# Kernel optimization log

Measured on AMD Instinct MI355X. Metric: run time of the kernel, lower is better.

## Reference

```python
import jax, jax.numpy as jnp
import numpy as np

N_HEADS = 12
LN_EPS = 1e-12


def _attention(x, mask, wq, bq, wk, bk, wv, bv, wo, bo):
    # standard BERT self-attention block (QKV + output projection, no LN here)
    B, S, D = x.shape
    Dh = D // N_HEADS
    q = (x @ wq + bq).reshape(B, S, N_HEADS, Dh)
    k = (x @ wk + bk).reshape(B, S, N_HEADS, Dh)
    v = (x @ wv + bv).reshape(B, S, N_HEADS, Dh)
    scores = jnp.einsum('bqhd,bkhd->bhqk', q, k) / jnp.sqrt(jnp.asarray(Dh, x.dtype))
    scores = scores + mask[:, None, None, :]  # additive mask, broadcast over heads/queries
    a = jax.nn.softmax(scores, axis=-1)
    ctx = jnp.einsum('bhqk,bkhd->bqhd', a, v).reshape(B, S, D)
    return ctx @ wo + bo


def _ffn(x, w1, b1, w2, b2):
    return jax.nn.gelu(x @ w1 + b1, approximate=False) @ w2 + b2


def _switch_ffn(x, wr, br, w1, b1, w2, b2):
    # token-level top-1 Switch FFN: route each token, scale output by max route prob.
    # All sub-experts are computed densely and combined with a one-hot mask so the
    # math is identical to gather/scatter dispatch but jit-friendly.
    B, S, D = x.shape
    E = wr.shape[-1]
    tok = x.reshape(-1, D)  # [N, D]
    p = jax.nn.softmax(tok @ wr + br, axis=-1)  # [N, E]
    pmax = p.max(axis=-1)
    oh = jax.nn.one_hot(p.argmax(axis=-1), E, dtype=tok.dtype)  # [N, E]
    h = jax.nn.gelu(jnp.einsum('nd,edf->enf', tok, w1) + b1[:, None, :], approximate=False)
    y = jnp.einsum('enf,efd->end', h, w2) + b2[:, None, :]  # [E, N, D]
    out = jnp.einsum('ne,end->nd', oh, y) * pmax[:, None]
    return out.reshape(B, S, D)


def setup_inputs() -> dict:
    B, S, D, F, U, E = 16, 128, 768, 3072, 4, 4
    key = jax.random.key(0)
    ks = jax.random.split(key, 20)
    w = lambda i, sh: jax.random.normal(ks[i], sh, dtype=jnp.float32) * 0.02
    z = lambda sh: jnp.zeros(sh, jnp.float32)
    return {
        'x': jax.random.normal(ks[0], (B, S, D), jnp.float32),
        'attn_mask': z((B, S)),
        'sw_w': w(1, (D, U)), 'sw_b': z((U,)),
        'ca_wq': w(2, (D, D)), 'ca_bq': z((D,)),
        'ca_wk': w(3, (D, D)), 'ca_bk': z((D,)),
        'ca_wv': w(4, (D, D)), 'ca_bv': z((D,)),
        'ca_wo': w(5, (D, D)), 'ca_bo': z((D,)),
        'ua_wq': w(6, (U, D, D)), 'ua_bq': z((U, D)),
        'ua_wk': w(7, (U, D, D)), 'ua_bk': z((U, D)),
        'ua_wv': w(8, (U, D, D)), 'ua_bv': z((U, D)),
        'ua_wo': w(9, (U, D, D)), 'ua_bo': z((U, D)),
        'cf_w1': w(10, (D, F)), 'cf_b1': z((F,)),
        'cf_w2': w(11, (F, D)), 'cf_b2': z((D,)),
        'ur_w': w(12, (U, D, E)), 'ur_b': z((U, E)),
        'uf_w1': w(13, (U, E, D, F)), 'uf_b1': z((U, E, F)),
        'uf_w2': w(14, (U, E, F, D)), 'uf_b2': z((U, E, D)),
        'ln_g': jnp.ones((D,), jnp.float32), 'ln_b': z((D,)),
    }


def reference(x, attn_mask, sw_w, sw_b,
              ca_wq, ca_bq, ca_wk, ca_bk, ca_wv, ca_bv, ca_wo, ca_bo,
              ua_wq, ua_bq, ua_wk, ua_bk, ua_wv, ua_bv, ua_wo, ua_bo,
              cf_w1, cf_b1, cf_w2, cf_b2,
              ur_w, ur_b, uf_w1, uf_b1, uf_w2, uf_b2,
              ln_g, ln_b):
    U = sw_w.shape[-1]
    # common attention expert (full batch)
    common_attn = _attention(x, attn_mask, ca_wq, ca_bq, ca_wk, ca_bk, ca_wv, ca_bv, ca_wo, ca_bo)
    # batch-level routing: mean-pool over sequence, softmax + top-1
    route_p = jax.nn.softmax(x.mean(axis=1) @ sw_w + sw_b, axis=-1)  # [B, U]
    pmax = route_p.max(axis=-1)    # [B]
    routes = route_p.argmax(axis=-1)  # [B]
    # unique attention experts: masked dense compute == gather/scatter by batch row
    unique_attn = jnp.zeros_like(x)
    for i in range(U):
        sel = (routes == i)[:, None, None]
        out_i = _attention(x, attn_mask, ua_wq[i], ua_bq[i], ua_wk[i], ua_bk[i],
                           ua_wv[i], ua_bv[i], ua_wo[i], ua_bo[i])
        unique_attn = unique_attn + jnp.where(sel, out_i, jnp.zeros((), x.dtype))
    # note: original multiplies ONLY the unique branch by route_prob_max
    att = common_attn + pmax[:, None, None] * unique_attn
    # unique Switch-FFN experts (token-level top-1 inside each unique expert)
    unique_ffn = jnp.zeros_like(x)
    for i in range(U):
        sel = (routes == i)[:, None, None]
        out_i = _switch_ffn(att, ur_w[i], ur_b[i], uf_w1[i], uf_b1[i], uf_w2[i], uf_b2[i])
        unique_ffn = unique_ffn + jnp.where(sel, out_i, jnp.zeros((), x.dtype))
    common_ffn = _ffn(att, cf_w1, cf_b1, cf_w2, cf_b2)
    ffn_out = common_ffn + unique_ffn  # dropout in eval mode == identity
    y = att + ffn_out
    mu = y.mean(axis=-1, keepdims=True)
    var = y.var(axis=-1, keepdims=True)
    return (y - mu) / jnp.sqrt(var + LN_EPS) * ln_g + ln_b
```

## Files before the change

kernel.cpp:

```cpp
#include <hip/hip_runtime.h>

#define NT 2048
#define Dm 768
#define Fm 3072
#define Bm 16
#define Sm 128
#define Hm 12
#define DHm 64

#define BM 64
#define BM2 128
#define BN 128
#define BK 32

typedef __attribute__((ext_vector_type(8))) short bf16x8;
typedef __attribute__((ext_vector_type(4))) float f32x4;

__device__ __forceinline__ unsigned short f2bf(float f){
  unsigned u = __float_as_uint(f);
  unsigned r = (u + 0x7fffu + ((u>>16)&1u)) >> 16;
  return (unsigned short)r;
}
__device__ __forceinline__ float bf2f(unsigned short h){ return __uint_as_float(((unsigned)h)<<16); }
__device__ __forceinline__ unsigned fsplit2(float x){
  unsigned short h = f2bf(x);
  unsigned short l = f2bf(x - bf2f(h));
  return (unsigned)h | ((unsigned)l << 16);
}
__device__ __forceinline__ void bsplit2(float a, float b, unsigned &hi2, unsigned &lo2){
  asm("v_cvt_pk_bf16_f32 %0, %1, %2" : "=v"(hi2) : "v"(a), "v"(b));
  float fa = __uint_as_float(hi2 << 16);
  float fb = __uint_as_float(hi2 & 0xffff0000u);
  asm("v_cvt_pk_bf16_f32 %0, %1, %2" : "=v"(lo2) : "v"(a - fa), "v"(b - fb));
}
__device__ __forceinline__ float gelu_f(float x){
  return 0.5f*x*(1.0f + erff(x*0.70710678118654752f));
}

__device__ __forceinline__ void mm_tile2(
    const short* __restrict__ Abf, int lda,
    const int* __restrict__ gidx, int m0, int mbound,
    const float* __restrict__ W0, int N, int K, int n0,
    f32x4 acc[4][4])
{
  int lane = threadIdx.x & 63, wv = threadIdx.x >> 6;
  int wm = wv & 1, wn = wv >> 1;
  int oct = lane >> 4, l16 = lane & 15;
  const short* aptr[4];
  #pragma unroll
  for(int fi=0; fi<4; fi++){
    int lr = wm*64 + fi*16 + l16;
    int grow = (lr < mbound) ? (gidx ? gidx[m0 + lr] : (m0 + lr)) : -1;
    aptr[fi] = (grow >= 0) ? (Abf + (size_t)grow*lda + oct*8) : nullptr;
  }
  const float* bptr[4];
  #pragma unroll
  for(int fj=0; fj<4; fj++)
    bptr[fj] = W0 + (size_t)(oct*8)*N + (n0 + wn*64 + fj*16 + l16);

  const bf16x8 zz = {0,0,0,0,0,0,0,0};
  bf16x8 av[4]; float bw[4][8];
  #pragma unroll
  for(int fi=0; fi<4; fi++) av[fi] = aptr[fi] ? *(const bf16x8*)(aptr[fi]) : zz;
  #pragma unroll
  for(int fj=0; fj<4; fj++)
    #pragma unroll
    for(int i=0;i<8;i++) bw[fj][i] = bptr[fj][(size_t)i*N];

  for(int k0=0; k0<K; k0+=BK){
    bf16x8 af[4];
    #pragma unroll
    for(int fi=0; fi<4; fi++) af[fi] = av[fi];
    bf16x8 bfr[4];
    #pragma unroll
    for(int fj=0; fj<4; fj++){
      unsigned o0,o1,o2,o3;
      asm("v_cvt_pk_bf16_f32 %0, %1, %2" : "=v"(o0) : "v"(bw[fj][0]), "v"(bw[fj][1]));
      asm("v_cvt_pk_bf16_f32 %0, %1, %2" : "=v"(o1) : "v"(bw[fj][2]), "v"(bw[fj][3]));
      asm("v_cvt_pk_bf16_f32 %0, %1, %2" : "=v"(o2) : "v"(bw[fj][4]), "v"(bw[fj][5]));
      asm("v_cvt_pk_bf16_f32 %0, %1, %2" : "=v"(o3) : "v"(bw[fj][6]), "v"(bw[fj][7]));
      union{ bf16x8 v; unsigned u[4]; } r;
      r.u[0]=o0; r.u[1]=o1; r.u[2]=o2; r.u[3]=o3;
      bfr[fj] = r.v;
    }
    if(k0+BK < K){
      int kn = k0 + BK;
      #pragma unroll
      for(int fi=0; fi<4; fi++) av[fi] = aptr[fi] ? *(const bf16x8*)(aptr[fi] + kn) : zz;
      #pragma unroll
      for(int fj=0; fj<4; fj++)
        #pragma unroll
        for(int i=0;i<8;i++) bw[fj][i] = bptr[fj][(size_t)(kn + i)*N];
    }
    __builtin_amdgcn_s_setprio(1);
    #pragma unroll
    for(int fi=0; fi<4; fi++)
      #pragma unroll
      for(int fj=0; fj<4; fj++)
        acc[fi][fj] = __builtin_amdgcn_mfma_f32_16x16x32_bf16(af[fi], bfr[fj], acc[fi][fj], 0, 0, 0);
    __builtin_amdgcn_s_setprio(0);
  }
}

__device__ __forceinline__ void mm_tile3b(
    const short* __restrict__ Ahi, const short* __restrict__ Alo, int lda, int m0, int acol,
    const float* __restrict__ W0, int N, int K, int n0,
    f32x4 acc[2][4])
{
  int lane = threadIdx.x & 63, wv = threadIdx.x >> 6;
  int wm = wv & 1, wn = wv >> 1;
  int oct = lane >> 4, l16 = lane & 15;
  size_t aoffs[2];
  #pragma unroll
  for(int fi=0; fi<2; fi++){
    int lr = wm*32 + fi*16 + l16;
    aoffs[fi] = (size_t)(m0 + lr)*lda + acol + oct*8;
  }
  const float* bptr[4];
  #pragma unroll
  for(int fj=0; fj<4; fj++)
    bptr[fj] = W0 + (size_t)(oct*8)*N + (n0 + wn*64 + fj*16 + l16);

  bf16x8 avH[2], avL[2]; float bw[4][8];
  #pragma unroll
  for(int fi=0; fi<2; fi++){
    avH[fi] = *(const bf16x8*)(Ahi + aoffs[fi]);
    avL[fi] = *(const bf16x8*)(Alo + aoffs[fi]);
  }
  #pragma unroll
  for(int fj=0; fj<4; fj++)
    #pragma unroll
    for(int i=0;i<8;i++) bw[fj][i] = bptr[fj][(size_t)i*N];

  for(int k0=0; k0<K; k0+=BK){
    bf16x8 ah[2], al[2];
    #pragma unroll
    for(int fi=0; fi<2; fi++){ ah[fi]=avH[fi]; al[fi]=avL[fi]; }
    bf16x8 bh[4], bl[4];
    #pragma unroll
    for(int fj=0; fj<4; fj++){
      unsigned h0,l0,h1,l1,h2,l2,h3,l3;
      bsplit2(bw[fj][0], bw[fj][1], h0, l0);
      bsplit2(bw[fj][2], bw[fj][3], h1, l1);
      bsplit2(bw[fj][4], bw[fj][5], h2, l2);
      bsplit2(bw[fj][6], bw[fj][7], h3, l3);
      union{ bf16x8 v; unsigned u[4]; } rh, rl;
      rh.u[0]=h0; rh.u[1]=h1; rh.u[2]=h2; rh.u[3]=h3;
      rl.u[0]=l0; rl.u[1]=l1; rl.u[2]=l2; rl.u[3]=l3;
      bh[fj] = rh.v; bl[fj] = rl.v;
    }
    if(k0+BK < K){
      int kn = k0 + BK;
      #pragma unroll
      for(int fi=0; fi<2; fi++){
        avH[fi] = *(const bf16x8*)(Ahi + aoffs[fi] + kn);
        avL[fi] = *(const bf16x8*)(Alo + aoffs[fi] + kn);
      }
      #pragma unroll
      for(int fj=0; fj<4; fj++)
        #pragma unroll
        for(int i=0;i<8;i++) bw[fj][i] = bptr[fj][(size_t)(kn + i)*N];
    }
    __builtin_amdgcn_s_setprio(1);
    #pragma unroll
    for(int fi=0; fi<2; fi++)
      #pragma unroll
      for(int fj=0; fj<4; fj++){
        acc[fi][fj] = __builtin_amdgcn_mfma_f32_16x16x32_bf16(ah[fi], bh[fj], acc[fi][fj], 0, 0, 0);
        acc[fi][fj] = __builtin_amdgcn_mfma_f32_16x16x32_bf16(ah[fi], bl[fj], acc[fi][fj], 0, 0, 0);
        acc[fi][fj] = __builtin_amdgcn_mfma_f32_16x16x32_bf16(al[fi], bh[fj], acc[fi][fj], 0, 0, 0);
      }
    __builtin_amdgcn_s_setprio(0);
  }
}

__global__ __launch_bounds__(256) void k_split_x(const float* __restrict__ in,
    short* __restrict__ hi, short* __restrict__ lo, int n4){
  int i = blockIdx.x*256 + threadIdx.x;
  if(i < n4){
    float4 v = ((const float4*)in)[i];
    unsigned h01,l01,h23,l23;
    bsplit2(v.x, v.y, h01, l01);
    bsplit2(v.z, v.w, h23, l23);
    short4 h, l;
    h.x=(short)(h01&0xffff); h.y=(short)(h01>>16); h.z=(short)(h23&0xffff); h.w=(short)(h23>>16);
    l.x=(short)(l01&0xffff); l.y=(short)(l01>>16); l.z=(short)(l23&0xffff); l.w=(short)(l23>>16);
    ((short4*)hi)[i] = h;
    ((short4*)lo)[i] = l;
  }
}

struct PtrArr6 { const float* w[6]; const float* b[6]; };

__global__ __launch_bounds__(256) void mm3_qkv(const short* __restrict__ x_hi,
    const short* __restrict__ x_lo, PtrArr6 pa,
    const int* __restrict__ routeb, float* __restrict__ qkvout)
{
  int n0 = blockIdx.x*BN, m0 = blockIdx.y*BM, z = blockIdx.z;
  int bidx = m0 >> 7;
  const float* W = pa.w[z]; const float* bias = pa.b[z];
  if(z >= 3){ int e = routeb[bidx]; W += (size_t)e*Dm*Dm; bias += (size_t)e*Dm; }
  f32x4 acc[2][4] = {};
  mm_tile3b(x_hi, x_lo, Dm, m0, 0, W, Dm, Dm, n0, acc);
  float* outp = qkvout + (size_t)z*NT*Dm;
  int lane = threadIdx.x&63, wv = threadIdx.x>>6, wm = wv&1, wn = wv>>1;
  #pragma unroll
  for(int fi=0; fi<2; fi++)
    #pragma unroll
    for(int fj=0; fj<4; fj++)
      #pragma unroll
      for(int r=0; r<4; r++){
        int row = m0 + wm*32 + fi*16 + ((lane>>4)<<2) + r;
        int col = n0 + wn*64 + fj*16 + (lane&15);
        outp[(size_t)row*Dm + col] = acc[fi][fj][r] + bias[col];
      }
}

__global__ __launch_bounds__(256) void mm3_outproj(const short* __restrict__ ctx_hi,
    const short* __restrict__ ctx_lo,
    const float* __restrict__ ca_wo, const float* __restrict__ ua_wo,
    const float* __restrict__ ca_bo, const float* __restrict__ ua_bo,
    const int* __restrict__ routeb, const float* __restrict__ pmaxb,
    float* __restrict__ att4)
{
  const int KC = Dm/2;
  int n0 = blockIdx.x*BN, m0 = blockIdx.y*BM, kc = blockIdx.z;
  int bidx = m0 >> 7;
  int e = routeb[bidx];
  int uq = kc >> 1, kh = kc & 1;
  const float* Wb = uq ? (ua_wo + (size_t)e*Dm*Dm) : ca_wo;
  const float* W  = Wb + (size_t)kh*KC*Dm;
  int acol = uq*Dm + kh*KC;
  f32x4 acc[2][4] = {};
  mm_tile3b(ctx_hi, ctx_lo, 1536, m0, acol, W, Dm, KC, n0, acc);
  float* outp = att4 + (size_t)kc*NT*Dm;
  int lane = threadIdx.x&63, wv = threadIdx.x>>6, wm = wv&1, wn = wv>>1;
  #pragma unroll
  for(int fi=0; fi<2; fi++)
    #pragma unroll
    for(int fj=0; fj<4; fj++)
      #pragma unroll
      for(int r=0; r<4; r++){
        int row = m0 + wm*32 + fi*16 + ((lane>>4)<<2) + r;
        int col = n0 + wn*64 + fj*16 + (lane&15);
        float bv = 0.f;
        if(kh == 0) bv = uq ? pmaxb[bidx]*ua_bo[(size_t)e*Dm + col] : ca_bo[col];
        outp[(size_t)row*Dm + col] = acc[fi][fj][r] + bv;
      }
}

__global__ __launch_bounds__(256) void k_att_sum(const float* __restrict__ att4,
    float* __restrict__ att, short* __restrict__ attbf, int n4){
  int i = blockIdx.x*256 + threadIdx.x;
  if(i < n4){
    const size_t P4 = (size_t)NT*Dm/4;
    float4 a = ((const float4*)att4)[i];
    float4 b = ((const float4*)att4)[P4 + i];
    float4 c = ((const float4*)att4)[2*P4 + i];
    float4 d = ((const float4*)att4)[3*P4 + i];
    float4 v;
    v.x=a.x+b.x+c.x+d.x; v.y=a.y+b.y+c.y+d.y;
    v.z=a.z+b.z+c.z+d.z; v.w=a.w+b.w+c.w+d.w;
    ((float4*)att)[i] = v;
    short4 o;
    o.x=(short)f2bf(v.x); o.y=(short)f2bf(v.y); o.z=(short)f2bf(v.z); o.w=(short)f2bf(v.w);
    ((short4*)attbf)[i] = o;
  }
}

__global__ __launch_bounds__(256) void mm_fstage(const short* __restrict__ attbf,
    const float* __restrict__ cf_w1, const float* __restrict__ cf_b1,
    const float* __restrict__ uf_w1, const float* __restrict__ uf_b1,
    const int* __restrict__ idxl, const int* __restrict__ gbase, const int* __restrict__ gcnt,
    const int* __restrict__ tlist, const int* __restrict__ ntl,
    short* __restrict__ h, short* __restrict__ hg)
{
  int n0 = blockIdx.x*BN, y = blockIdx.y;
  int lane = threadIdx.x&63, wv = threadIdx.x>>6, wm = wv&1, wn = wv>>1;
  f32x4 acc[4][4] = {};
  if(y < 16){
    int m0 = y*BM2;
    mm_tile2(attbf, Dm, nullptr, m0, BM2, cf_w1, Fm, Dm, n0, acc);
    #pragma unroll
    for(int fi=0; fi<4; fi++)
      #pragma unroll
      for(int fj=0; fj<4; fj++)
        #pragma unroll
        for(int r=0; r<4; r++){
          int row = m0 + wm*64 + fi*16 + ((lane>>4)<<2) + r;
          int col = n0 + wn*64 + fj*16 + (lane&15);
          h[(size_t)row*Fm + col] = (short)f2bf(gelu_f(acc[fi][fj][r] + cf_b1[col]));
        }
  } else {
    int i = y - 16;
    if(i >= ntl[0]) return;
    int v = tlist[i], g = v>>8, t = v&255;
    int cnt = gcnt[g], r0 = t*BM2, pos0 = gbase[g] + r0;
    mm_tile2(attbf, Dm, idxl, pos0, cnt - r0, uf_w1 + (size_t)g*Dm*Fm, Fm, Dm, n0, acc);
    const float* bias = uf_b1 + (size_t)g*Fm;
    #pragma unroll
    for(int fi=0; fi<4; fi++)
      #pragma unroll
      for(int fj=0; fj<4; fj++)
        #pragma unroll
        for(int r=0; r<4; r++){
          int lr = wm*64 + fi*16 + ((lane>>4)<<2) + r;
          if(r0 + lr >= cnt) continue;
          int col = n0 + wn*64 + fj*16 + (lane&15);
          hg[(size_t)(pos0+lr)*Fm + col] = (short)f2bf(gelu_f(acc[fi][fj][r] + bias[col]));
        }
  }
}

__global__ __launch_bounds__(256) void mm_dstage(const short* __restrict__ h,
    const short* __restrict__ hg,
    const float* __restrict__ cf_w2, const float* __restrict__ cf_b2,
    const float* __restrict__ uf_w2, const float* __restrict__ uf_b2,
    const int* __restrict__ idxl, const int* __restrict__ gbase, const int* __restrict__ gcnt,
    const int* __restrict__ tlist, const int* __restrict__ ntl,
    const float* __restrict__ tokp, short* __restrict__ ycf4, short* __restrict__ yuo4)
{
  const int KC = Fm/4;
  int bx = blockIdx.x;
  int n0 = (bx % 6)*BN, kc = bx / 6;
  int y = blockIdx.y;
  int lane = threadIdx.x&63, wv = threadIdx.x>>6, wm = wv&1, wn = wv>>1;
  f32x4 acc[4][4] = {};
  if(y < 16){
    int m0 = y*BM2;
    mm_tile2(h + kc*KC, Fm, nullptr, m0, BM2, cf_w2 + (size_t)kc*KC*Dm, Dm, KC, n0, acc);
    short* outp = ycf4 + (size_t)kc*NT*Dm;
    #pragma unroll
    for(int fi=0; fi<4; fi++)
      #pragma unroll
      for(int fj=0; fj<4; fj++)
        #pragma unroll
        for(int r=0; r<4; r++){
          int row = m0 + wm*64 + fi*16 + ((lane>>4)<<2) + r;
          int col = n0 + wn*64 + fj*16 + (lane&15);
          outp[(size_t)row*Dm + col] = (short)f2bf(acc[fi][fj][r] + (kc==0 ? cf_b2[col] : 0.f));
        }
  } else {
    int i = y - 16;
    if(i >= ntl[0]) return;
    int v = tlist[i], g = v>>8, t = v&255;
    int cnt = gcnt[g], r0 = t*BM2, pos0 = gbase[g] + r0;
    mm_tile2(hg + kc*KC, Fm, nullptr, pos0, cnt - r0,
             uf_w2 + (size_t)g*Fm*Dm + (size_t)kc*KC*Dm, Dm, KC, n0, acc);
    const float* bias = uf_b2 + (size_t)g*Dm;
    short* outp = yuo4 + (size_t)kc*NT*Dm;
    #pragma unroll
    for(int fi=0; fi<4; fi++)
      #pragma unroll
      for(int fj=0; fj<4; fj++)
        #pragma unroll
        for(int r=0; r<4; r++){
          int lr = wm*64 + fi*16 + ((lane>>4)<<2) + r;
          int rm = (r0 + lr < cnt) ? idxl[pos0 + lr] : -1;
          if(rm < 0) continue;
          int col = n0 + wn*64 + fj*16 + (lane&15);
          float vv = acc[fi][fj][r] + (kc==0 ? bias[col] : 0.f);
          outp[(size_t)rm*Dm + col] = (short)f2bf(vv * tokp[rm]);
        }
  }
}

__global__ __launch_bounds__(256) void k_route_batch(const float* __restrict__ xf,
    const float* __restrict__ sw_w, const float* __restrict__ sw_b,
    float* __restrict__ pmax_b, int* __restrict__ route_b){
  int b = blockIdx.x, tid = threadIdx.x;
  __shared__ float xm[Dm];
  for(int d=tid; d<Dm; d+=256){
    float s=0.f;
    const float* xp = xf + ((size_t)b*Sm)*Dm + d;
    for(int ss=0; ss<Sm; ss++) s += xp[(size_t)ss*Dm];
    xm[d] = s*(1.0f/Sm);
  }
  __syncthreads();
  float a0=0,a1=0,a2=0,a3=0;
  for(int d=tid; d<Dm; d+=256){
    float xv = xm[d];
    a0 += xv*sw_w[d*4+0]; a1 += xv*sw_w[d*4+1];
    a2 += xv*sw_w[d*4+2]; a3 += xv*sw_w[d*4+3];
  }
  __shared__ float red[4][256];
  red[0][tid]=a0; red[1][tid]=a1; red[2][tid]=a2; red[3][tid]=a3;
  for(int off=128; off>0; off>>=1){
    __syncthreads();
    if(tid<off){ for(int u=0;u<4;u++) red[u][tid]+=red[u][tid+off]; }
  }
  __syncthreads();
  if(tid==0){
    float l[4]; for(int u=0;u<4;u++) l[u]=red[u][0]+sw_b[u];
    float m=l[0]; int arg=0;
    for(int u=1;u<4;u++) if(l[u]>m){ m=l[u]; arg=u; }
    float s=0; for(int u=0;u<4;u++) s+=expf(l[u]-m);
    pmax_b[b]=1.0f/s;
    route_b[b]=arg;
  }
}

__global__ __launch_bounds__(256) void k_attn_f(const float* __restrict__ qkv,
    const float* __restrict__ mask, const float* __restrict__ pmaxb,
    short* __restrict__ ctx_hi, short* __restrict__ ctx_lo)
{
  int h = blockIdx.x, b = blockIdx.y, z = blockIdx.z;
  int qh = z & 1, kind = z >> 1;
  const float* Q  = qkv + (size_t)(kind*3+0)*NT*Dm;
  const float* Kp = qkv + (size_t)(kind*3+1)*NT*Dm;
  const float* Vp = qkv + (size_t)(kind*3+2)*NT*Dm;
  int tid = threadIdx.x;
  __shared__ float kv[128][68];
  size_t base = ((size_t)b*Sm)*Dm + h*DHm;
  for(int l=tid; l<2048; l+=256){
    int s=l>>4, d4=(l&15)*4;
    *(float4*)&kv[s][d4] = *(const float4*)(Kp + base + (size_t)s*Dm + d4);
  }
  int ql = tid>>2, quarter = tid&3;
  int qi = qh*64 + ql;
  float4 q4[16];
  const float* qp = Q + base + (size_t)qi*Dm;
  #pragma unroll
  for(int j=0;j<16;j++) q4[j] = *(const float4*)(qp + j*4);
  __syncthreads();
  float sc[32];
  #pragma unroll 4
  for(int t=0;t<32;t++){
    int ki = quarter + 4*t;
    float s=0.f;
    #pragma unroll
    for(int j=0;j<16;j++){
      float4 k4 = *(float4*)&kv[ki][j*4];
      s += q4[j].x*k4.x + q4[j].y*k4.y + q4[j].z*k4.z + q4[j].w*k4.w;
    }
    sc[t] = s*0.125f + mask[b*Sm+ki];
  }
  float m = sc[0];
  #pragma unroll
  for(int t=1;t<32;t++) m = fmaxf(m, sc[t]);
  m = fmaxf(m, __shfl_xor(m,1));
  m = fmaxf(m, __shfl_xor(m,2));
  float sum = 0.f;
  #pragma unroll
  for(int t=0;t<32;t++){ sc[t] = expf(sc[t]-m); sum += sc[t]; }
  sum += __shfl_xor(sum,1);
  sum += __shfl_xor(sum,2);
  float inv = 1.0f/sum;
  #pragma unroll
  for(int t=0;t<32;t++) sc[t] *= inv;
  __syncthreads();
  for(int l=tid; l<2048; l+=256){
    int s=l>>4, d4=(l&15)*4;
    *(float4*)&kv[s][d4] = *(const float4*)(Vp + base + (size_t)s*Dm + d4);
  }
  __syncthreads();
  float4 part[16];
  #pragma unroll
  for(int j=0;j<16;j++){ part[j].x=0; part[j].y=0; part[j].z=0; part[j].w=0; }
  #pragma unroll 4
  for(int t=0;t<32;t++){
    int ki = quarter + 4*t;
    float p = sc[t];
    #pragma unroll
    for(int j=0;j<16;j++){
      float4 v4 = *(float4*)&kv[ki][j*4];
      part[j].x += p*v4.x; part[j].y += p*v4.y; part[j].z += p*v4.z; part[j].w += p*v4.w;
    }
  }
  #pragma unroll
  for(int j=0;j<16;j++){
    part[j].x += __shfl_xor(part[j].x,1); part[j].x += __shfl_xor(part[j].x,2);
    part[j].y += __shfl_xor(part[j].y,1); part[j].y += __shfl_xor(part[j].y,2);
    part[j].z += __shfl_xor(part[j].z,1); part[j].z += __shfl_xor(part[j].z,2);
    part[j].w += __shfl_xor(part[j].w,1); part[j].w += __shfl_xor(part[j].w,2);
  }
  float sck = kind ? pmaxb[b] : 1.0f;
  size_t obase = ((size_t)b*Sm + qi)*1536 + kind*Dm + h*DHm;
  #pragma unroll
  for(int jj=0;jj<4;jj++){
    int j = quarter*4 + jj;
    float4 v = part[j];
    v.x *= sck; v.y *= sck; v.z *= sck; v.w *= sck;
    short4 hh, ll;
    unsigned short t0;
    t0=f2bf(v.x); hh.x=(short)t0; ll.x=(short)f2bf(v.x-bf2f(t0));
    t0=f2bf(v.y); hh.y=(short)t0; ll.y=(short)f2bf(v.y-bf2f(t0));
    t0=f2bf(v.z); hh.z=(short)t0; ll.z=(short)f2bf(v.z-bf2f(t0));
    t0=f2bf(v.w); hh.w=(short)t0; ll.w=(short)f2bf(v.w-bf2f(t0));
    *(short4*)(ctx_hi + obase + j*4) = hh;
    *(short4*)(ctx_lo + obase + j*4) = ll;
  }
}

__global__ __launch_bounds__(256) void k_tok_route(const float* __restrict__ att,
    const float* __restrict__ ur_w, const float* __restrict__ ur_b,
    const int* __restrict__ route_b, float* __restrict__ tok_pmax,
    int* __restrict__ tok_e, int* __restrict__ grp_count)
{
  int n = blockIdx.x, tid = threadIdx.x;
  int i = route_b[n>>7];
  const float* w = ur_w + (size_t)i*Dm*4;
  const float* ap = att + (size_t)n*Dm;
  float a0=0,a1=0,a2=0,a3=0;
  for(int d=tid; d<Dm; d+=256){
    float a = ap[d];
    a0 += a*w[d*4+0]; a1 += a*w[d*4+1];
    a2 += a*w[d*4+2]; a3 += a*w[d*4+3];
  }
  __shared__ float red[4][256];
  red[0][tid]=a0; red[1][tid]=a1; red[2][tid]=a2; red[3][tid]=a3;
  for(int off=128; off>0; off>>=1){
    __syncthreads();
    if(tid<off){ for(int u=0;u<4;u++) red[u][tid]+=red[u][tid+off]; }
  }
  __syncthreads();
  if(tid==0){
    float l[4]; for(int u=0;u<4;u++) l[u]=red[u][0]+ur_b[i*4+u];
    float m=l[0]; int arg=0;
    for(int u=1;u<4;u++) if(l[u]>m){ m=l[u]; arg=u; }
    float s=0; for(int u=0;u<4;u++) s+=expf(l[u]-m);
    tok_pmax[n] = 1.0f/s;
    tok_e[n] = arg;
    atomicAdd(&grp_count[i*4+arg], 1);
  }
}

__global__ void k_prefix(const int* __restrict__ cnt, int* __restrict__ base,
                         int* __restrict__ cur, int* __restrict__ tlist, int* __restrict__ ntl){
  if(threadIdx.x==0 && blockIdx.x==0){
    int s=0, nt=0;
    for(int g=0; g<16; g++){
      base[g]=s; cur[g]=s;
      int tg = (cnt[g] + BM2 - 1)/BM2;
      for(int t=0; t<tg; t++){ if(nt<32) tlist[nt++] = (g<<8)|t; }
      s += cnt[g];
    }
    ntl[0] = nt;
  }
}

__global__ void k_scatter(const int* __restrict__ route_b, const int* __restrict__ tok_e,
                          int* __restrict__ cur, int* __restrict__ idxl){
  int n = blockIdx.x*256 + threadIdx.x;
  if(n < NT){
    int g = route_b[n>>7]*4 + tok_e[n];
    int pos = atomicAdd(&cur[g], 1);
    idxl[pos] = n;
  }
}

__global__ __launch_bounds__(256) void k_final_ln(const float* __restrict__ att,
    const short* __restrict__ ycf4, const short* __restrict__ yuo4,
    const float* __restrict__ ln_g, const float* __restrict__ ln_b, float* __restrict__ out)
{
  int n = blockIdx.x, tid = threadIdx.x;
  __shared__ float yb[Dm];
  __shared__ float red[256];
  size_t base = (size_t)n*Dm;
  const size_t P = (size_t)NT*Dm;
  float ps = 0.f;
  for(int d=tid; d<Dm; d+=256){
    float v = att[base+d];
    #pragma unroll
    for(int c=0; c<4; c++){
      v += bf2f((unsigned short)ycf4[c*P + base + d]);
      v += bf2f((unsigned short)yuo4[c*P + base + d]);
    }
    yb[d]=v; ps+=v;
  }
  red[tid]=ps;
  for(int off=128; off>0; off>>=1){ __syncthreads(); if(tid<off) red[tid]+=red[tid+off]; }
  __syncthreads();
  float mu = red[0]*(1.0f/Dm);
  __syncthreads();
  float pv = 0.f;
  for(int d=tid; d<Dm; d+=256){ float t = yb[d]-mu; pv += t*t; }
  red[tid]=pv;
  for(int off=128; off>0; off>>=1){ __syncthreads(); if(tid<off) red[tid]+=red[tid+off]; }
  __syncthreads();
  float var = red[0]*(1.0f/Dm);
  float rstd = rsqrtf(var + 1e-12f);
  for(int d=tid; d<Dm; d+=256){
    out[base+d] = (yb[d]-mu)*rstd*ln_g[d] + ln_b[d];
  }
}

extern "C" void kernel_launch(void* const* d_in, const int* in_sizes, int n_in,
                              void* d_out, int out_size, void* d_ws, size_t ws_size,
                              hipStream_t stream)
{
  const float* x     =(const float*)d_in[0];
  const float* mask  =(const float*)d_in[1];
  const float* sw_w  =(const float*)d_in[2];
  const float* sw_b  =(const float*)d_in[3];
  const float* ca_wq =(const float*)d_in[4];
  const float* ca_bq =(const float*)d_in[5];
  const float* ca_wk =(const float*)d_in[6];
  const float* ca_bk =(const float*)d_in[7];
  const float* ca_wv =(const float*)d_in[8];
  const float* ca_bv =(const float*)d_in[9];
  const float* ca_wo =(const float*)d_in[10];
  const float* ca_bo =(const float*)d_in[11];
  const float* ua_wq =(const float*)d_in[12];
  const float* ua_bq =(const float*)d_in[13];
  const float* ua_wk =(const float*)d_in[14];
  const float* ua_bk =(const float*)d_in[15];
  const float* ua_wv =(const float*)d_in[16];
  const float* ua_bv =(const float*)d_in[17];
  const float* ua_wo =(const float*)d_in[18];
  const float* ua_bo =(const float*)d_in[19];
  const float* cf_w1 =(const float*)d_in[20];
  const float* cf_b1 =(const float*)d_in[21];
  const float* cf_w2 =(const float*)d_in[22];
  const float* cf_b2 =(const float*)d_in[23];
  const float* ur_w  =(const float*)d_in[24];
  const float* ur_b  =(const float*)d_in[25];
  const float* uf_w1 =(const float*)d_in[26];
  const float* uf_b1 =(const float*)d_in[27];
  const float* uf_w2 =(const float*)d_in[28];
  const float* uf_b2 =(const float*)d_in[29];
  const float* ln_g  =(const float*)d_in[30];
  const float* ln_b  =(const float*)d_in[31];

  float* region = (float*)d_ws;
  float* qkv    = region;
  short* ctx_hi = (short*)(region + (size_t)6*NT*Dm);
  short* ctx_lo = (short*)(region + (size_t)7*NT*Dm);
  float* att4   = region;
  short* h_bf   = (short*)region;
  short* hg_bf  = (short*)region + (size_t)NT*Fm;
  short* ycf4   = (short*)(region + (size_t)4*NT*Dm);
  short* yuo4   = (short*)(region + (size_t)6*NT*Dm);
  float* fp     = region + (size_t)8*NT*Dm;
  short* x_hi   = (short*)fp;
  short* x_lo   = x_hi + (size_t)NT*Dm;
  float* att    = fp; fp += (size_t)NT*Dm;
  float* tokp   = fp; fp += NT;
  float* pmaxb  = fp; fp += 16;
  short* att_bf = (short*)fp;
  int*   ip     = (int*)(att_bf + (size_t)NT*Dm);
  int* routeb = ip; ip += 16;
  int* toke   = ip; ip += NT;
  int* gcnt   = ip; ip += 16;
  int* gbase  = ip; ip += 16;
  int* gcur   = ip; ip += 16;
  int* idxl   = ip; ip += NT;
  int* tlist  = ip; ip += 64;
  int* ntl    = ip; ip += 1;
  size_t need = (size_t)((char*)ip - (char*)d_ws);
  if(need > ws_size) return;

  (void)hipMemsetAsync(gcnt, 0, 16*sizeof(int), stream);

  k_route_batch<<<16, 256, 0, stream>>>(x, sw_w, sw_b, pmaxb, routeb);
  k_split_x<<<(NT*Dm/4 + 255)/256, 256, 0, stream>>>(x, x_hi, x_lo, NT*Dm/4);

  PtrArr6 pa;
  pa.w[0]=ca_wq; pa.w[1]=ca_wk; pa.w[2]=ca_wv; pa.w[3]=ua_wq; pa.w[4]=ua_wk; pa.w[5]=ua_wv;
  pa.b[0]=ca_bq; pa.b[1]=ca_bk; pa.b[2]=ca_bv; pa.b[3]=ua_bq; pa.b[4]=ua_bk; pa.b[5]=ua_bv;
  mm3_qkv<<<dim3(Dm/BN, NT/BM, 6), 256, 0, stream>>>(x_hi, x_lo, pa, routeb, qkv);

  k_attn_f<<<dim3(Hm, Bm, 4), 256, 0, stream>>>(qkv, mask, pmaxb, ctx_hi, ctx_lo);

  mm3_outproj<<<dim3(Dm/BN, NT/BM, 4), 256, 0, stream>>>(ctx_hi, ctx_lo, ca_wo, ua_wo,
                                                         ca_bo, ua_bo, routeb, pmaxb, att4);
  k_att_sum<<<(NT*Dm/4 + 255)/256, 256, 0, stream>>>(att4, att, att_bf, NT*Dm/4);

  k_tok_route<<<NT, 256, 0, stream>>>(att, ur_w, ur_b, routeb, tokp, toke, gcnt);
  k_prefix<<<1, 64, 0, stream>>>(gcnt, gbase, gcur, tlist, ntl);
  k_scatter<<<NT/256, 256, 0, stream>>>(routeb, toke, gcur, idxl);

  mm_fstage<<<dim3(Fm/BN, 16+32), 256, 0, stream>>>(att_bf, cf_w1, cf_b1, uf_w1, uf_b1,
                                                    idxl, gbase, gcnt, tlist, ntl, h_bf, hg_bf);

  mm_dstage<<<dim3(24, 16+32), 256, 0, stream>>>(h_bf, hg_bf, cf_w2, cf_b2, uf_w2, uf_b2,
                                                 idxl, gbase, gcnt, tlist, ntl, tokp,
                                                 ycf4, yuo4);

  k_final_ln<<<NT, 256, 0, stream>>>(att, ycf4, yuo4, ln_g, ln_b, (float*)d_out);
}
```

Measured before the change: 547.9 us.

## Split-K the first FFN GEMM stage and combine partials with GELU

The first FFN projection, both the common path and the grouped unique-expert path, is split into two K-halves along a new grid z dimension. Each half writes bf16 partial sums, with the bias added only by the first half. A new elementwise kernel then adds the two partials and applies GELU before the second GEMM. The aim is more blocks in flight and shorter per-block K loops. The cost is extra global memory traffic, two extra launches, and an added bf16 rounding of the partial sums before the GELU.

```diff
diff --git a/kernel.cpp b/kernel.cpp
--- a/kernel.cpp
+++ b/kernel.cpp
@@ -273,14 +273,16 @@
     const float* __restrict__ uf_w1, const float* __restrict__ uf_b1,
     const int* __restrict__ idxl, const int* __restrict__ gbase, const int* __restrict__ gcnt,
     const int* __restrict__ tlist, const int* __restrict__ ntl,
-    short* __restrict__ h, short* __restrict__ hg)
-{
-  int n0 = blockIdx.x*BN, y = blockIdx.y;
+    short* __restrict__ hp, short* __restrict__ hgp)
+{
+  const int KC = Dm/2;
+  int n0 = blockIdx.x*BN, y = blockIdx.y, kc = blockIdx.z;
   int lane = threadIdx.x&63, wv = threadIdx.x>>6, wm = wv&1, wn = wv>>1;
   f32x4 acc[4][4] = {};
   if(y < 16){
     int m0 = y*BM2;
-    mm_tile2(attbf, Dm, nullptr, m0, BM2, cf_w1, Fm, Dm, n0, acc);
+    mm_tile2(attbf + kc*KC, Dm, nullptr, m0, BM2, cf_w1 + (size_t)kc*KC*Fm, Fm, KC, n0, acc);
+    short* outp = hp + (size_t)kc*NT*Fm;
     #pragma unroll
     for(int fi=0; fi<4; fi++)
       #pragma unroll
@@ -289,15 +291,17 @@
         for(int r=0; r<4; r++){
           int row = m0 + wm*64 + fi*16 + ((lane>>4)<<2) + r;
           int col = n0 + wn*64 + fj*16 + (lane&15);
-          h[(size_t)row*Fm + col] = (short)f2bf(gelu_f(acc[fi][fj][r] + cf_b1[col]));
+          outp[(size_t)row*Fm + col] = (short)f2bf(acc[fi][fj][r] + (kc==0 ? cf_b1[col] : 0.f));
         }
   } else {
     int i = y - 16;
     if(i >= ntl[0]) return;
     int v = tlist[i], g = v>>8, t = v&255;
     int cnt = gcnt[g], r0 = t*BM2, pos0 = gbase[g] + r0;
-    mm_tile2(attbf, Dm, idxl, pos0, cnt - r0, uf_w1 + (size_t)g*Dm*Fm, Fm, Dm, n0, acc);
+    mm_tile2(attbf + kc*KC, Dm, idxl, pos0, cnt - r0,
+             uf_w1 + (size_t)g*Dm*Fm + (size_t)kc*KC*Fm, Fm, KC, n0, acc);
     const float* bias = uf_b1 + (size_t)g*Fm;
+    short* outp = hgp + (size_t)kc*NT*Fm;
     #pragma unroll
     for(int fi=0; fi<4; fi++)
       #pragma unroll
@@ -307,8 +311,23 @@
           int lr = wm*64 + fi*16 + ((lane>>4)<<2) + r;
           if(r0 + lr >= cnt) continue;
           int col = n0 + wn*64 + fj*16 + (lane&15);
-          hg[(size_t)(pos0+lr)*Fm + col] = (short)f2bf(gelu_f(acc[fi][fj][r] + bias[col]));
+          outp[(size_t)(pos0+lr)*Fm + col] = (short)f2bf(acc[fi][fj][r] + (kc==0 ? bias[col] : 0.f));
         }
+  }
+}
+
+__global__ __launch_bounds__(256) void k_hcombine(const short* __restrict__ c1,
+    short* __restrict__ c0out, int n4){
+  int i = blockIdx.x*256 + threadIdx.x;
+  if(i < n4){
+    short4 a = ((const short4*)c0out)[i];
+    short4 b = ((const short4*)c1)[i];
+    short4 o;
+    o.x = (short)f2bf(gelu_f(bf2f((unsigned short)a.x) + bf2f((unsigned short)b.x)));
+    o.y = (short)f2bf(gelu_f(bf2f((unsigned short)a.y) + bf2f((unsigned short)b.y)));
+    o.z = (short)f2bf(gelu_f(bf2f((unsigned short)a.z) + bf2f((unsigned short)b.z)));
+    o.w = (short)f2bf(gelu_f(bf2f((unsigned short)a.w) + bf2f((unsigned short)b.w)));
+    ((short4*)c0out)[i] = o;
   }
 }
 
@@ -627,9 +646,9 @@
   short* ctx_hi = (short*)(region + (size_t)6*NT*Dm);
   short* ctx_lo = (short*)(region + (size_t)7*NT*Dm);
   float* att4   = region;
-  short* h_bf   = (short*)region;
-  short* hg_bf  = (short*)region + (size_t)NT*Fm;
-  short* ycf4   = (short*)(region + (size_t)4*NT*Dm);
+  short* hp     = (short*)region;
+  short* hgp    = (short*)(region + (size_t)4*NT*Dm);
+  short* ycf4   = (short*)(region + (size_t)2*NT*Dm);
   short* yuo4   = (short*)(region + (size_t)6*NT*Dm);
   float* fp     = region + (size_t)8*NT*Dm;
   short* x_hi   = (short*)fp;
@@ -670,10 +689,12 @@
   k_prefix<<<1, 64, 0, stream>>>(gcnt, gbase, gcur, tlist, ntl);
   k_scatter<<<NT/256, 256, 0, stream>>>(routeb, toke, gcur, idxl);
 
-  mm_fstage<<<dim3(Fm/BN, 16+32), 256, 0, stream>>>(att_bf, cf_w1, cf_b1, uf_w1, uf_b1,
-                                                    idxl, gbase, gcnt, tlist, ntl, h_bf, hg_bf);
-
-  mm_dstage<<<dim3(24, 16+32), 256, 0, stream>>>(h_bf, hg_bf, cf_w2, cf_b2, uf_w2, uf_b2,
+  mm_fstage<<<dim3(Fm/BN, 16+32, 2), 256, 0, stream>>>(att_bf, cf_w1, cf_b1, uf_w1, uf_b1,
+                                                       idxl, gbase, gcnt, tlist, ntl, hp, hgp);
+  k_hcombine<<<(NT*Fm/4 + 255)/256, 256, 0, stream>>>(hp + (size_t)NT*Fm, hp, NT*Fm/4);
+  k_hcombine<<<(NT*Fm/4 + 255)/256, 256, 0, stream>>>(hgp + (size_t)NT*Fm, hgp, NT*Fm/4);
+
+  mm_dstage<<<dim3(24, 16+32), 256, 0, stream>>>(hp, hgp, cf_w2, cf_b2, uf_w2, uf_b2,
                                                  idxl, gbase, gcnt, tlist, ntl, tokp,
                                                  ycf4, yuo4);
 
```

Result: slower. 575.1 us (+5.0%).
